# Optimization experiments

Hardware: AMD Instinct MI355X
Metric: run time of the kernel (lower is better)

## Reference

```python
import jax, jax.numpy as jnp
import numpy as np

NUM_HEADS = 32
HEAD_DIM = 32  # hard-coded in the module


def _rope_sincos(seq_len, head_dim):
    # NOTE: module uses arange(0, head_dim)/head_dim (full dim, not the usual /2 stride)
    inv_freq = 1.0 / (10000.0 ** (jnp.arange(0, head_dim, dtype=jnp.float32) / head_dim))
    freqs = jnp.outer(jnp.arange(seq_len, dtype=jnp.float32), inv_freq)  # [S, D]
    # original repeats over heads then reshapes -> identical values per head,
    # so broadcasting with shape [1, S, 1, D] is equivalent.
    return jnp.sin(freqs)[None, :, None, :], jnp.cos(freqs)[None, :, None, :]


def _apply_rope(x, sin, cos):
    x1, x2 = jnp.split(x, 2, axis=-1)
    x_rot = jnp.concatenate([-x2, x1], axis=-1)
    return x * cos + x_rot * sin


def setup_inputs() -> dict:
    key = jax.random.key(0)
    B, S, H, D = 2, 2048, NUM_HEADS, HEAD_DIM
    dm = H * D
    k1, k2 = jax.random.split(key)
    x = jax.random.normal(k1, (B, S, dm), dtype=jnp.float32)
    W_qkv = jax.random.normal(k2, (dm, 3 * dm), dtype=jnp.float32) / np.sqrt(dm).astype(np.float32)
    mask = jnp.tril(jnp.ones((S, S), dtype=bool))[None, None]  # causal, [1,1,S,S]
    return {"x": x, "W_qkv": W_qkv, "mask": mask}


def reference(x, W_qkv, mask):
    B, S, dm = x.shape
    H, D = NUM_HEADS, HEAD_DIM
    qkv = x @ W_qkv  # [B, S, 3*H*D], no bias
    q, k, v = jnp.split(qkv, 3, axis=-1)
    q = q.reshape(B, S, H, D)
    k = k.reshape(B, S, H, D)
    v = v.reshape(B, S, H, D)

    sin, cos = _rope_sincos(S, D)
    q = _apply_rope(q, sin, cos)
    k = _apply_rope(k, sin, cos)

    # [B, H, S, D]
    q = q.transpose(0, 2, 1, 3)
    k = k.transpose(0, 2, 1, 3)
    v = v.transpose(0, 2, 1, 3)

    scale = 1.0 / np.sqrt(D).astype(np.float32)
    attn = jnp.einsum('bhqd,bhkd->bhqk', q, k) * scale  # [B, H, S, S]
    attn = jnp.where(mask, attn, jnp.float32(-jnp.inf))
    attn = jax.nn.softmax(attn, axis=-1)
    out = jnp.einsum('bhqk,bhkd->bhqd', attn, v)  # [B, H, S, D]
    return out.transpose(0, 2, 1, 3).reshape(B, S, H * D)
```

## Files before the change

### kernel.cpp

```cpp
#include <hip/hip_runtime.h>
#include <cstdint>
#include <cstddef>

#define BB 2
#define SS 2048
#define HH 32
#define DD 32
#define DM 1024
#define MROWS 4096
#define NQKV 3072

#define QSCALE 0.25503486f

typedef __attribute__((ext_vector_type(8))) short bf16x8;
typedef __attribute__((ext_vector_type(4))) float f32x4;
typedef __attribute__((address_space(1))) unsigned int gu32;
typedef __attribute__((address_space(3))) unsigned int lu32;

__device__ __forceinline__ unsigned short f2bf(float f) {
    union { float f; unsigned int u; } v;
    v.f = f;
    unsigned int u = v.u;
    u += 0x7fffu + ((u >> 16) & 1u);
    return (unsigned short)(u >> 16);
}

__device__ __forceinline__ unsigned int cvt_pk_bf16(float a, float b) {
    unsigned int r;
    asm("v_cvt_pk_bf16_f32 %0, %1, %2" : "=v"(r) : "v"(a), "v"(b));
    return r;
}
__device__ __forceinline__ unsigned short bf1(float a) {
    return (unsigned short)cvt_pk_bf16(a, a);
}

__global__ __launch_bounds__(256) void prep_k(
        const float* __restrict__ x, const float* __restrict__ w,
        unsigned short* __restrict__ xb, unsigned short* __restrict__ wT,
        float* __restrict__ tk, float* __restrict__ tq) {
    __shared__ unsigned short tile[64][65];
    const int blk = blockIdx.x;
    const int tid = threadIdx.x;
    if (blk < 4096) {
        const int i = blk * 256 + tid;
        float4 v = ((const float4*)x)[i];
        ushort4 o;
        o.x = f2bf(v.x); o.y = f2bf(v.y); o.z = f2bf(v.z); o.w = f2bf(v.w);
        ((ushort4*)xb)[i] = o;
    } else if (blk < 4864) {
        const int bx = blk - 4096;
        const int n0 = (bx % 48) * 64;
        const int k0 = (bx / 48) * 64;
        const int tx = tid & 63;
        const int ty = tid >> 6;
        for (int i = ty; i < 64; i += 4)
            tile[i][tx] = f2bf(w[(size_t)(k0 + i) * NQKV + n0 + tx]);
        __syncthreads();
        for (int i = ty; i < 64; i += 4)
            wT[(size_t)(n0 + i) * 1024 + k0 + tx] = tile[tx][i];
    } else {
        const int i = (blk - 4864) * 256 + tid;
        const int s = i >> 4, dl = i & 15;
        const float inv1 = exp2f((float)dl * -0.41524101186092029f);
        const float inv2 = exp2f((float)(dl + 16) * -0.41524101186092029f);
        float s1, c1, s2, c2;
        sincosf((float)s * inv1, &s1, &c1);
        sincosf((float)s * inv2, &s2, &c2);
        float4 vk = {s1, c1, s2, c2};
        float4 vq = {s1 * QSCALE, c1 * QSCALE, s2 * QSCALE, c2 * QSCALE};
        ((float4*)tk)[i] = vk;
        ((float4*)tq)[i] = vq;
    }
}

__global__ __launch_bounds__(256) void qkv_gemm_k(
        const unsigned short* __restrict__ xb,
        const unsigned short* __restrict__ wTp,
        const float4* __restrict__ tk, const float4* __restrict__ tq,
        unsigned short* __restrict__ qbuf,
        unsigned short* __restrict__ kbuf,
        unsigned short* __restrict__ vtbuf) {
    __shared__ unsigned short smem[2 * 128 * 32];
    unsigned short* As = smem;
    unsigned short* Bs = smem + 4096;
    const int m0 = blockIdx.x * 128;
    const int n0 = blockIdx.y * 128;
    const int tid = threadIdx.x;
    const int w = tid >> 6, lane = tid & 63;
    const int quad = lane >> 4, l16 = lane & 15;
    const int wr = w >> 1, wc = w & 1;

    f32x4 acc[4][4];
#pragma unroll
    for (int i = 0; i < 4; ++i)
#pragma unroll
        for (int j = 0; j < 4; ++j)
            acc[i][j] = (f32x4){0.f, 0.f, 0.f, 0.f};

    const int G = (lane & 56) | ((lane ^ (lane >> 3)) & 7);
    const int goff = (G >> 2) * 1024 + (G & 3) * 8;
    const int Gr = l16 * 4 + quad;
    const int L = Gr ^ ((Gr >> 3) & 7);
    const int roff = L * 8;

    for (int k0 = 0; k0 < 1024; k0 += 32) {
        __syncthreads();
#pragma unroll
        for (int q = 0; q < 2; ++q) {
            const int seg = w * 2 + q;
            const unsigned short* ga = xb  + (size_t)(m0 + seg * 16) * 1024 + k0 + goff;
            const unsigned short* gb = wTp + (size_t)(n0 + seg * 16) * 1024 + k0 + goff;
            __builtin_amdgcn_global_load_lds((gu32*)ga, (lu32*)(As + seg * 512), 16, 0, 0);
            __builtin_amdgcn_global_load_lds((gu32*)gb, (lu32*)(Bs + seg * 512), 16, 0, 0);
        }
        __syncthreads();
        bf16x8 af[4], bfv[4];
#pragma unroll
        for (int i = 0; i < 4; ++i)
            af[i] = *(const bf16x8*)(As + (wr * 4 + i) * 512 + roff);
#pragma unroll
        for (int j = 0; j < 4; ++j)
            bfv[j] = *(const bf16x8*)(Bs + (wc * 4 + j) * 512 + roff);
#pragma unroll
        for (int i = 0; i < 4; ++i)
#pragma unroll
            for (int j = 0; j < 4; ++j)
                acc[i][j] = __builtin_amdgcn_mfma_f32_16x16x32_bf16(af[i], bfv[j], acc[i][j], 0, 0, 0);
    }

    const int sec = n0 >> 10;
    const int rowb = m0 + wr * 64;
    const int colb = n0 + wc * 64;
    if (sec < 2) {
        unsigned short* dst = (sec == 0) ? qbuf : kbuf;
        const float4* tab = (sec == 0) ? tq : tk;
        const int h0 = (colb & 1023) >> 5;
        const int h1 = ((colb + 32) & 1023) >> 5;
#pragma unroll
        for (int i = 0; i < 4; ++i) {
#pragma unroll
            for (int r = 0; r < 4; ++r) {
                const int row = rowb + i * 16 + quad * 4 + r;
                const int bb = row >> 11, s = row & 2047;
                const float4 t = tab[s * 16 + l16];
                unsigned short* pb = dst + ((size_t)(bb * 32) * 2048 + s) * 32;
                {
                    const float x1 = acc[i][0][r], x2 = acc[i][1][r];
                    unsigned short* p = pb + (size_t)h0 * (2048 * 32);
                    p[l16]      = bf1(x1 * t.y - x2 * t.x);
                    p[l16 + 16] = bf1(x2 * t.w + x1 * t.z);
                }
                {
                    const float x1 = acc[i][2][r], x2 = acc[i][3][r];
                    unsigned short* p = pb + (size_t)h1 * (2048 * 32);
                    p[l16]      = bf1(x1 * t.y - x2 * t.x);
                    p[l16 + 16] = bf1(x2 * t.w + x1 * t.z);
                }
            }
        }
    } else {
        __syncthreads();
        unsigned short* tw = smem + w * 2048;
        const int bbi = rowb >> 11;
        const int srow = rowb & 2047;
        const int colB = colb - 2048;
#pragma unroll
        for (int j = 0; j < 4; ++j) {
#pragma unroll
            for (int i = 0; i < 4; ++i) {
                uint2 pk;
                pk.x = cvt_pk_bf16(acc[i][j][0], acc[i][j][1]);
                pk.y = cvt_pk_bf16(acc[i][j][2], acc[i][j][3]);
                *(uint2*)&tw[l16 * 66 + i * 16 + quad * 4] = pk;
            }
#pragma unroll
            for (int c = 0; c < 16; ++c) {
                const int col = colB + j * 16 + c;
                const int hh = col >> 5, d = col & 31;
                vtbuf[((size_t)(bbi * 32 + hh) * 32 + d) * 2048 + srow + lane] = tw[c * 66 + lane];
            }
        }
    }
}

__global__ __launch_bounds__(256) void attn_k(
        const unsigned short* __restrict__ qb,
        const unsigned short* __restrict__ kb,
        const unsigned short* __restrict__ vt,
        float* __restrict__ out) {
    __shared__ unsigned short Pl[4][2][32][40];
    const int tid = threadIdx.x;
    const int w = tid >> 6, lane = tid & 63;
    const int quad = lane >> 4, l16 = lane & 15;
    const int bh = blockIdx.x >> 3;
    const int pr = blockIdx.x & 7;
    const int b = bh >> 5, h = bh & 31;

    const unsigned short* qbase = qb + (size_t)bh * 2048 * 32;
    const unsigned short* kbase = kb + (size_t)bh * 2048 * 32;
    const unsigned short* vbase = vt + (size_t)bh * 32 * 2048;
    const f32x4 fz = {0.f, 0.f, 0.f, 0.f};

    for (int ph = 0; ph < 2; ++ph) {
        const int qw = (ph == 0) ? (pr * 128 + w * 32)
                                 : ((15 - pr) * 128 + (3 - w) * 32);
        const int nkt = (qw >> 5) + 1;

        bf16x8 qf0 = *(const bf16x8*)(qbase + (size_t)(qw + l16) * 32 + quad * 8);
        bf16x8 qf1 = *(const bf16x8*)(qbase + (size_t)(qw + 16 + l16) * 32 + quad * 8);

        f32x4 a00 = fz, a01 = fz, a10 = fz, a11 = fz;
        float ls0 = 0.f, ls1 = 0.f;

        const unsigned short* kp0 = kbase + (size_t)l16 * 32 + quad * 8;
        const unsigned short* kp1 = kbase + (size_t)(16 + l16) * 32 + quad * 8;
        const unsigned short* vp0 = vbase + (size_t)l16 * 2048 + quad * 8;
        const unsigned short* vp1 = vbase + (size_t)(16 + l16) * 2048 + quad * 8;

        bf16x8 kc0 = *(const bf16x8*)kp0;
        bf16x8 kc1 = *(const bf16x8*)kp1;
        bf16x8 vc0 = *(const bf16x8*)vp0;
        bf16x8 vc1 = *(const bf16x8*)vp1;

        for (int kt = 0; kt < nkt - 1; ++kt) {
            kp0 += 1024; kp1 += 1024; vp0 += 32; vp1 += 32;
            bf16x8 kn0 = *(const bf16x8*)kp0;
            bf16x8 kn1 = *(const bf16x8*)kp1;
            bf16x8 vn0 = *(const bf16x8*)vp0;
            bf16x8 vn1 = *(const bf16x8*)vp1;

            f32x4 s00 = __builtin_amdgcn_mfma_f32_16x16x32_bf16(kc0, qf0, fz, 0, 0, 0);
            f32x4 s01 = __builtin_amdgcn_mfma_f32_16x16x32_bf16(kc0, qf1, fz, 0, 0, 0);
            f32x4 s10 = __builtin_amdgcn_mfma_f32_16x16x32_bf16(kc1, qf0, fz, 0, 0, 0);
            f32x4 s11 = __builtin_amdgcn_mfma_f32_16x16x32_bf16(kc1, qf1, fz, 0, 0, 0);

            unsigned short (*plw)[40] = Pl[w][kt & 1];
            {
                float p0 = __builtin_amdgcn_exp2f(s00[0]), p1 = __builtin_amdgcn_exp2f(s00[1]);
                float p2 = __builtin_amdgcn_exp2f(s00[2]), p3 = __builtin_amdgcn_exp2f(s00[3]);
                ls0 += (p0 + p1) + (p2 + p3);
                uint2 pk; pk.x = cvt_pk_bf16(p0, p1); pk.y = cvt_pk_bf16(p2, p3);
                *(uint2*)&plw[l16][quad * 4] = pk;
            }
            {
                float p0 = __builtin_amdgcn_exp2f(s01[0]), p1 = __builtin_amdgcn_exp2f(s01[1]);
                float p2 = __builtin_amdgcn_exp2f(s01[2]), p3 = __builtin_amdgcn_exp2f(s01[3]);
                ls1 += (p0 + p1) + (p2 + p3);
                uint2 pk; pk.x = cvt_pk_bf16(p0, p1); pk.y = cvt_pk_bf16(p2, p3);
                *(uint2*)&plw[16 + l16][quad * 4] = pk;
            }
            {
                float p0 = __builtin_amdgcn_exp2f(s10[0]), p1 = __builtin_amdgcn_exp2f(s10[1]);
                float p2 = __builtin_amdgcn_exp2f(s10[2]), p3 = __builtin_amdgcn_exp2f(s10[3]);
                ls0 += (p0 + p1) + (p2 + p3);
                uint2 pk; pk.x = cvt_pk_bf16(p0, p1); pk.y = cvt_pk_bf16(p2, p3);
                *(uint2*)&plw[l16][16 + quad * 4] = pk;
            }
            {
                float p0 = __builtin_amdgcn_exp2f(s11[0]), p1 = __builtin_amdgcn_exp2f(s11[1]);
                float p2 = __builtin_amdgcn_exp2f(s11[2]), p3 = __builtin_amdgcn_exp2f(s11[3]);
                ls1 += (p0 + p1) + (p2 + p3);
                uint2 pk; pk.x = cvt_pk_bf16(p0, p1); pk.y = cvt_pk_bf16(p2, p3);
                *(uint2*)&plw[16 + l16][16 + quad * 4] = pk;
            }

            bf16x8 pf0 = *(const bf16x8*)&plw[l16][quad * 8];
            bf16x8 pf1 = *(const bf16x8*)&plw[16 + l16][quad * 8];
            a00 = __builtin_amdgcn_mfma_f32_16x16x32_bf16(vc0, pf0, a00, 0, 0, 0);
            a01 = __builtin_amdgcn_mfma_f32_16x16x32_bf16(vc0, pf1, a01, 0, 0, 0);
            a10 = __builtin_amdgcn_mfma_f32_16x16x32_bf16(vc1, pf0, a10, 0, 0, 0);
            a11 = __builtin_amdgcn_mfma_f32_16x16x32_bf16(vc1, pf1, a11, 0, 0, 0);

            kc0 = kn0; kc1 = kn1; vc0 = vn0; vc1 = vn1;
        }

        {
            f32x4 s00 = __builtin_amdgcn_mfma_f32_16x16x32_bf16(kc0, qf0, fz, 0, 0, 0);
            f32x4 s01 = __builtin_amdgcn_mfma_f32_16x16x32_bf16(kc0, qf1, fz, 0, 0, 0);
            f32x4 s11 = __builtin_amdgcn_mfma_f32_16x16x32_bf16(kc1, qf1, fz, 0, 0, 0);

            unsigned short (*plw)[40] = Pl[w][(nkt - 1) & 1];
            {
                float p[4];
#pragma unroll
                for (int r = 0; r < 4; ++r)
                    p[r] = (quad * 4 + r > l16) ? 0.f : __builtin_amdgcn_exp2f(s00[r]);
                ls0 += (p[0] + p[1]) + (p[2] + p[3]);
                uint2 pk; pk.x = cvt_pk_bf16(p[0], p[1]); pk.y = cvt_pk_bf16(p[2], p[3]);
                *(uint2*)&plw[l16][quad * 4] = pk;
            }
            {
                float p0 = __builtin_amdgcn_exp2f(s01[0]), p1 = __builtin_amdgcn_exp2f(s01[1]);
                float p2 = __builtin_amdgcn_exp2f(s01[2]), p3 = __builtin_amdgcn_exp2f(s01[3]);
                ls1 += (p0 + p1) + (p2 + p3);
                uint2 pk; pk.x = cvt_pk_bf16(p0, p1); pk.y = cvt_pk_bf16(p2, p3);
                *(uint2*)&plw[16 + l16][quad * 4] = pk;
            }
            {
                uint2 pk; pk.x = 0; pk.y = 0;
                *(uint2*)&plw[l16][16 + quad * 4] = pk;
            }
            {
                float p[4];
#pragma unroll
                for (int r = 0; r < 4; ++r)
                    p[r] = (quad * 4 + r > l16) ? 0.f : __builtin_amdgcn_exp2f(s11[r]);
                ls1 += (p[0] + p[1]) + (p[2] + p[3]);
                uint2 pk; pk.x = cvt_pk_bf16(p[0], p[1]); pk.y = cvt_pk_bf16(p[2], p[3]);
                *(uint2*)&plw[16 + l16][16 + quad * 4] = pk;
            }

            bf16x8 pf0 = *(const bf16x8*)&plw[l16][quad * 8];
            bf16x8 pf1 = *(const bf16x8*)&plw[16 + l16][quad * 8];
            a00 = __builtin_amdgcn_mfma_f32_16x16x32_bf16(vc0, pf0, a00, 0, 0, 0);
            a01 = __builtin_amdgcn_mfma_f32_16x16x32_bf16(vc0, pf1, a01, 0, 0, 0);
            a10 = __builtin_amdgcn_mfma_f32_16x16x32_bf16(vc1, pf0, a10, 0, 0, 0);
            a11 = __builtin_amdgcn_mfma_f32_16x16x32_bf16(vc1, pf1, a11, 0, 0, 0);
        }

        float l0 = ls0; l0 += __shfl_xor(l0, 16); l0 += __shfl_xor(l0, 32);
        float l1 = ls1; l1 += __shfl_xor(l1, 16); l1 += __shfl_xor(l1, 32);
        const float inv0 = 1.f / l0, inv1 = 1.f / l1;

        float* ot = (float*)&Pl[w][0][0][0];
        {
            f32x4 t;
            t = a00; t[0]*=inv0; t[1]*=inv0; t[2]*=inv0; t[3]*=inv0;
            *(f32x4*)&ot[(l16) * 36 + quad * 4] = t;
            t = a10; t[0]*=inv0; t[1]*=inv0; t[2]*=inv0; t[3]*=inv0;
            *(f32x4*)&ot[(l16) * 36 + 16 + quad * 4] = t;
            t = a01; t[0]*=inv1; t[1]*=inv1; t[2]*=inv1; t[3]*=inv1;
            *(f32x4*)&ot[(16 + l16) * 36 + quad * 4] = t;
            t = a11; t[0]*=inv1; t[1]*=inv1; t[2]*=inv1; t[3]*=inv1;
            *(f32x4*)&ot[(16 + l16) * 36 + 16 + quad * 4] = t;
        }
        const int dd = lane & 31, qpar = lane >> 5;
        float* ob = out + (size_t)(b * 2048 + qw) * 1024 + h * 32;
#pragma unroll
        for (int i2 = 0; i2 < 16; ++i2) {
            const int qloc = i2 * 2 + qpar;
            ob[(size_t)qloc * 1024 + dd] = ot[qloc * 36 + dd];
        }
    }
}

extern "C" void kernel_launch(void* const* d_in, const int* in_sizes, int n_in,
                              void* d_out, int out_size, void* d_ws, size_t ws_size,
                              hipStream_t stream) {
    (void)in_sizes; (void)n_in; (void)out_size; (void)ws_size;
    const float* x = (const float*)d_in[0];
    const float* wq = (const float*)d_in[1];
    float* out = (float*)d_out;

    unsigned short* xb = (unsigned short*)d_ws;
    unsigned short* wT = xb + (size_t)MROWS * DM;
    unsigned short* qb = wT + (size_t)NQKV * DM;
    unsigned short* kb = qb + (size_t)BB * HH * SS * DD;
    unsigned short* vt = kb + (size_t)BB * HH * SS * DD;
    float* tk = (float*)(vt + (size_t)BB * HH * SS * DD);
    float* tq = tk + (size_t)SS * 16 * 4;

    prep_k<<<dim3(4992), dim3(256), 0, stream>>>(x, wq, xb, wT, tk, tq);
    qkv_gemm_k<<<dim3(MROWS / 128, NQKV / 128), dim3(256), 0, stream>>>(
        xb, wT, (const float4*)tk, (const float4*)tq, qb, kb, vt);
    attn_k<<<dim3(BB * HH * 8), dim3(256), 0, stream>>>(qb, kb, vt, out);
}
```

Baseline: 182.3 us.

## Keep P in registers via 16-row query tiles, dropping LDS round-trip

```diff
diff --git a/kernel.cpp b/kernel.cpp
--- a/kernel.cpp
+++ b/kernel.cpp
@@ -188,159 +188,129 @@
         const unsigned short* __restrict__ kb,
         const unsigned short* __restrict__ vt,
         float* __restrict__ out) {
-    __shared__ unsigned short Pl[4][2][32][40];
     const int tid = threadIdx.x;
     const int w = tid >> 6, lane = tid & 63;
     const int quad = lane >> 4, l16 = lane & 15;
-    const int bh = blockIdx.x >> 3;
-    const int pr = blockIdx.x & 7;
+    const int bh = blockIdx.x >> 4;
+    const int pr = blockIdx.x & 15;
     const int b = bh >> 5, h = bh & 31;
+    const int W = pr * 4 + w;
 
     const unsigned short* qbase = qb + (size_t)bh * 2048 * 32;
     const unsigned short* kbase = kb + (size_t)bh * 2048 * 32;
     const unsigned short* vbase = vt + (size_t)bh * 32 * 2048;
     const f32x4 fz = {0.f, 0.f, 0.f, 0.f};
 
+    typedef union { unsigned int u[4]; uint2 d[2]; bf16x8 v; } pk8;
+
     for (int ph = 0; ph < 2; ++ph) {
-        const int qw = (ph == 0) ? (pr * 128 + w * 32)
-                                 : ((15 - pr) * 128 + (3 - w) * 32);
+        const int j = (ph == 0) ? W : (127 - W);
+        const int qw = j * 16;
         const int nkt = (qw >> 5) + 1;
 
-        bf16x8 qf0 = *(const bf16x8*)(qbase + (size_t)(qw + l16) * 32 + quad * 8);
-        bf16x8 qf1 = *(const bf16x8*)(qbase + (size_t)(qw + 16 + l16) * 32 + quad * 8);
-
-        f32x4 a00 = fz, a01 = fz, a10 = fz, a11 = fz;
-        float ls0 = 0.f, ls1 = 0.f;
+        bf16x8 qf = *(const bf16x8*)(qbase + (size_t)(qw + l16) * 32 + quad * 8);
+
+        f32x4 a0 = fz, a1 = fz;
+        float ls = 0.f;
 
         const unsigned short* kp0 = kbase + (size_t)l16 * 32 + quad * 8;
         const unsigned short* kp1 = kbase + (size_t)(16 + l16) * 32 + quad * 8;
-        const unsigned short* vp0 = vbase + (size_t)l16 * 2048 + quad * 8;
-        const unsigned short* vp1 = vbase + (size_t)(16 + l16) * 2048 + quad * 8;
+        const unsigned short* vq0 = vbase + (size_t)l16 * 2048 + quad * 4;
+        const unsigned short* vq1 = vbase + (size_t)(16 + l16) * 2048 + quad * 4;
 
         bf16x8 kc0 = *(const bf16x8*)kp0;
         bf16x8 kc1 = *(const bf16x8*)kp1;
-        bf16x8 vc0 = *(const bf16x8*)vp0;
-        bf16x8 vc1 = *(const bf16x8*)vp1;
+        uint2 v00 = *(const uint2*)vq0;
+        uint2 v01 = *(const uint2*)(vq0 + 16);
+        uint2 v10 = *(const uint2*)vq1;
+        uint2 v11 = *(const uint2*)(vq1 + 16);
 
         for (int kt = 0; kt < nkt - 1; ++kt) {
-            kp0 += 1024; kp1 += 1024; vp0 += 32; vp1 += 32;
+            kp0 += 1024; kp1 += 1024; vq0 += 32; vq1 += 32;
             bf16x8 kn0 = *(const bf16x8*)kp0;
             bf16x8 kn1 = *(const bf16x8*)kp1;
-            bf16x8 vn0 = *(const bf16x8*)vp0;
-            bf16x8 vn1 = *(const bf16x8*)vp1;
-
-            f32x4 s00 = __builtin_amdgcn_mfma_f32_16x16x32_bf16(kc0, qf0, fz, 0, 0, 0);
-            f32x4 s01 = __builtin_amdgcn_mfma_f32_16x16x32_bf16(kc0, qf1, fz, 0, 0, 0);
-            f32x4 s10 = __builtin_amdgcn_mfma_f32_16x16x32_bf16(kc1, qf0, fz, 0, 0, 0);
-            f32x4 s11 = __builtin_amdgcn_mfma_f32_16x16x32_bf16(kc1, qf1, fz, 0, 0, 0);
-
-            unsigned short (*plw)[40] = Pl[w][kt & 1];
+            uint2 n00 = *(const uint2*)vq0;
+            uint2 n01 = *(const uint2*)(vq0 + 16);
+            uint2 n10 = *(const uint2*)vq1;
+            uint2 n11 = *(const uint2*)(vq1 + 16);
+
+            f32x4 s0 = __builtin_amdgcn_mfma_f32_16x16x32_bf16(kc0, qf, fz, 0, 0, 0);
+            f32x4 s1 = __builtin_amdgcn_mfma_f32_16x16x32_bf16(kc1, qf, fz, 0, 0, 0);
+
+            pk8 pf;
             {
-                float p0 = __builtin_amdgcn_exp2f(s00[0]), p1 = __builtin_amdgcn_exp2f(s00[1]);
-                float p2 = __builtin_amdgcn_exp2f(s00[2]), p3 = __builtin_amdgcn_exp2f(s00[3]);
-                ls0 += (p0 + p1) + (p2 + p3);
-                uint2 pk; pk.x = cvt_pk_bf16(p0, p1); pk.y = cvt_pk_bf16(p2, p3);
-                *(uint2*)&plw[l16][quad * 4] = pk;
+                float p0 = __builtin_amdgcn_exp2f(s0[0]), p1 = __builtin_amdgcn_exp2f(s0[1]);
+                float p2 = __builtin_amdgcn_exp2f(s0[2]), p3 = __builtin_amdgcn_exp2f(s0[3]);
+                ls += (p0 + p1) + (p2 + p3);
+                pf.u[0] = cvt_pk_bf16(p0, p1);
+                pf.u[1] = cvt_pk_bf16(p2, p3);
             }
             {
-                float p0 = __builtin_amdgcn_exp2f(s01[0]), p1 = __builtin_amdgcn_exp2f(s01[1]);
-                float p2 = __builtin_amdgcn_exp2f(s01[2]), p3 = __builtin_amdgcn_exp2f(s01[3]);
-                ls1 += (p0 + p1) + (p2 + p3);
-                uint2 pk; pk.x = cvt_pk_bf16(p0, p1); pk.y = cvt_pk_bf16(p2, p3);
-                *(uint2*)&plw[16 + l16][quad * 4] = pk;
-            }
-            {
-                float p0 = __builtin_amdgcn_exp2f(s10[0]), p1 = __builtin_amdgcn_exp2f(s10[1]);
-                float p2 = __builtin_amdgcn_exp2f(s10[2]), p3 = __builtin_amdgcn_exp2f(s10[3]);
-                ls0 += (p0 + p1) + (p2 + p3);
-                uint2 pk; pk.x = cvt_pk_bf16(p0, p1); pk.y = cvt_pk_bf16(p2, p3);
-                *(uint2*)&plw[l16][16 + quad * 4] = pk;
-            }
-            {
-                float p0 = __builtin_amdgcn_exp2f(s11[0]), p1 = __builtin_amdgcn_exp2f(s11[1]);
-                float p2 = __builtin_amdgcn_exp2f(s11[2]), p3 = __builtin_amdgcn_exp2f(s11[3]);
-                ls1 += (p0 + p1) + (p2 + p3);
-                uint2 pk; pk.x = cvt_pk_bf16(p0, p1); pk.y = cvt_pk_bf16(p2, p3);
-                *(uint2*)&plw[16 + l16][16 + quad * 4] = pk;
-            }
-
-            bf16x8 pf0 = *(const bf16x8*)&plw[l16][quad * 8];
-            bf16x8 pf1 = *(const bf16x8*)&plw[16 + l16][quad * 8];
-            a00 = __builtin_amdgcn_mfma_f32_16x16x32_bf16(vc0, pf0, a00, 0, 0, 0);
-            a01 = __builtin_amdgcn_mfma_f32_16x16x32_bf16(vc0, pf1, a01, 0, 0, 0);
-            a10 = __builtin_amdgcn_mfma_f32_16x16x32_bf16(vc1, pf0, a10, 0, 0, 0);
-            a11 = __builtin_amdgcn_mfma_f32_16x16x32_bf16(vc1, pf1, a11, 0, 0, 0);
-
-            kc0 = kn0; kc1 = kn1; vc0 = vn0; vc1 = vn1;
+                float p0 = __builtin_amdgcn_exp2f(s1[0]), p1 = __builtin_amdgcn_exp2f(s1[1]);
+                float p2 = __builtin_amdgcn_exp2f(s1[2]), p3 = __builtin_amdgcn_exp2f(s1[3]);
+                ls += (p0 + p1) + (p2 + p3);
+                pf.u[2] = cvt_pk_bf16(p0, p1);
+                pf.u[3] = cvt_pk_bf16(p2, p3);
+            }
+            pk8 vc0, vc1;
+            vc0.d[0] = v00; vc0.d[1] = v01;
+            vc1.d[0] = v10; vc1.d[1] = v11;
+            a0 = __builtin_amdgcn_mfma_f32_16x16x32_bf16(vc0.v, pf.v, a0, 0, 0, 0);
+            a1 = __builtin_amdgcn_mfma_f32_16x16x32_bf16(vc1.v, pf.v, a1, 0, 0, 0);
+
+            kc0 = kn0; kc1 = kn1; v00 = n00; v01 = n01; v10 = n10; v11 = n11;
         }
 
         {
-            f32x4 s00 = __builtin_amdgcn_mfma_f32_16x16x32_bf16(kc0, qf0, fz, 0, 0, 0);
-            f32x4 s01 = __builtin_amdgcn_mfma_f32_16x16x32_bf16(kc0, qf1, fz, 0, 0, 0);
-            f32x4 s11 = __builtin_amdgcn_mfma_f32_16x16x32_bf16(kc1, qf1, fz, 0, 0, 0);
-
-            unsigned short (*plw)[40] = Pl[w][(nkt - 1) & 1];
-            {
+            f32x4 s0 = __builtin_amdgcn_mfma_f32_16x16x32_bf16(kc0, qf, fz, 0, 0, 0);
+            pk8 pf;
+            if (j & 1) {
+                f32x4 s1 = __builtin_amdgcn_mfma_f32_16x16x32_bf16(kc1, qf, fz, 0, 0, 0);
+                {
+                    float p0 = __builtin_amdgcn_exp2f(s0[0]), p1 = __builtin_amdgcn_exp2f(s0[1]);
+                    float p2 = __builtin_amdgcn_exp2f(s0[2]), p3 = __builtin_amdgcn_exp2f(s0[3]);
+                    ls += (p0 + p1) + (p2 + p3);
+                    pf.u[0] = cvt_pk_bf16(p0, p1);
+                    pf.u[1] = cvt_pk_bf16(p2, p3);
+                }
+                {
+                    float p[4];
+#pragma unroll
+                    for (int r = 0; r < 4; ++r)
+                        p[r] = (quad * 4 + r > l16) ? 0.f : __builtin_amdgcn_exp2f(s1[r]);
+                    ls += (p[0] + p[1]) + (p[2] + p[3]);
+                    pf.u[2] = cvt_pk_bf16(p[0], p[1]);
+                    pf.u[3] = cvt_pk_bf16(p[2], p[3]);
+                }
+            } else {
                 float p[4];
 #pragma unroll
                 for (int r = 0; r < 4; ++r)
-                    p[r] = (quad * 4 + r > l16) ? 0.f : __builtin_amdgcn_exp2f(s00[r]);
-                ls0 += (p[0] + p[1]) + (p[2] + p[3]);
-                uint2 pk; pk.x = cvt_pk_bf16(p[0], p[1]); pk.y = cvt_pk_bf16(p[2], p[3]);
-                *(uint2*)&plw[l16][quad * 4] = pk;
-            }
-            {
-                float p0 = __builtin_amdgcn_exp2f(s01[0]), p1 = __builtin_amdgcn_exp2f(s01[1]);
-                float p2 = __builtin_amdgcn_exp2f(s01[2]), p3 = __builtin_amdgcn_exp2f(s01[3]);
-                ls1 += (p0 + p1) + (p2 + p3);
-                uint2 pk; pk.x = cvt_pk_bf16(p0, p1); pk.y = cvt_pk_bf16(p2, p3);
-                *(uint2*)&plw[16 + l16][quad * 4] = pk;
-            }
-            {
-                uint2 pk; pk.x = 0; pk.y = 0;
-                *(uint2*)&plw[l16][16 + quad * 4] = pk;
-            }
-            {
-                float p[4];
-#pragma unroll
-                for (int r = 0; r < 4; ++r)
-                    p[r] = (quad * 4 + r > l16) ? 0.f : __builtin_amdgcn_exp2f(s11[r]);
-                ls1 += (p[0] + p[1]) + (p[2] + p[3]);
-                uint2 pk; pk.x = cvt_pk_bf16(p[0], p[1]); pk.y = cvt_pk_bf16(p[2], p[3]);
-                *(uint2*)&plw[16 + l16][16 + quad * 4] = pk;
-            }
-
-            bf16x8 pf0 = *(const bf16x8*)&plw[l16][quad * 8];
-            bf16x8 pf1 = *(const bf16x8*)&plw[16 + l16][quad * 8];
-            a00 = __builtin_amdgcn_mfma_f32_16x16x32_bf16(vc0, pf0, a00, 0, 0, 0);
-            a01 = __builtin_amdgcn_mfma_f32_16x16x32_bf16(vc0, pf1, a01, 0, 0, 0);
-            a10 = __builtin_amdgcn_mfma_f32_16x16x32_bf16(vc1, pf0, a10, 0, 0, 0);
-            a11 = __builtin_amdgcn_mfma_f32_16x16x32_bf16(vc1, pf1, a11, 0, 0, 0);
-        }
-
-        float l0 = ls0; l0 += __shfl_xor(l0, 16); l0 += __shfl_xor(l0, 32);
-        float l1 = ls1; l1 += __shfl_xor(l1, 16); l1 += __shfl_xor(l1, 32);
-        const float inv0 = 1.f / l0, inv1 = 1.f / l1;
-
-        float* ot = (float*)&Pl[w][0][0][0];
-        {
-            f32x4 t;
-            t = a00; t[0]*=inv0; t[1]*=inv0; t[2]*=inv0; t[3]*=inv0;
-            *(f32x4*)&ot[(l16) * 36 + quad * 4] = t;
-            t = a10; t[0]*=inv0; t[1]*=inv0; t[2]*=inv0; t[3]*=inv0;
-            *(f32x4*)&ot[(l16) * 36 + 16 + quad * 4] = t;
-            t = a01; t[0]*=inv1; t[1]*=inv1; t[2]*=inv1; t[3]*=inv1;
-            *(f32x4*)&ot[(16 + l16) * 36 + quad * 4] = t;
-            t = a11; t[0]*=inv1; t[1]*=inv1; t[2]*=inv1; t[3]*=inv1;
-            *(f32x4*)&ot[(16 + l16) * 36 + 16 + quad * 4] = t;
-        }
-        const int dd = lane & 31, qpar = lane >> 5;
-        float* ob = out + (size_t)(b * 2048 + qw) * 1024 + h * 32;
-#pragma unroll
-        for (int i2 = 0; i2 < 16; ++i2) {
-            const int qloc = i2 * 2 + qpar;
-            ob[(size_t)qloc * 1024 + dd] = ot[qloc * 36 + dd];
-        }
+                    p[r] = (quad * 4 + r > l16) ? 0.f : __builtin_amdgcn_exp2f(s0[r]);
+                ls += (p[0] + p[1]) + (p[2] + p[3]);
+                pf.u[0] = cvt_pk_bf16(p[0], p[1]);
+                pf.u[1] = cvt_pk_bf16(p[2], p[3]);
+                pf.u[2] = 0;
+                pf.u[3] = 0;
+            }
+            pk8 vc0, vc1;
+            vc0.d[0] = v00; vc0.d[1] = v01;
+            vc1.d[0] = v10; vc1.d[1] = v11;
+            a0 = __builtin_amdgcn_mfma_f32_16x16x32_bf16(vc0.v, pf.v, a0, 0, 0, 0);
+            a1 = __builtin_amdgcn_mfma_f32_16x16x32_bf16(vc1.v, pf.v, a1, 0, 0, 0);
+        }
+
+        float l = ls;
+        l += __shfl_xor(l, 16);
+        l += __shfl_xor(l, 32);
+        const float inv = 1.f / l;
+
+        float* ob = out + (size_t)(b * 2048 + qw + l16) * 1024 + h * 32 + quad * 4;
+        float4 o0, o1;
+        o0.x = a0[0] * inv; o0.y = a0[1] * inv; o0.z = a0[2] * inv; o0.w = a0[3] * inv;
+        o1.x = a1[0] * inv; o1.y = a1[1] * inv; o1.z = a1[2] * inv; o1.w = a1[3] * inv;
+        *(float4*)ob = o0;
+        *(float4*)(ob + 16) = o1;
     }
 }
 
@@ -363,5 +333,5 @@
     prep_k<<<dim3(4992), dim3(256), 0, stream>>>(x, wq, xb, wT, tk, tq);
     qkv_gemm_k<<<dim3(MROWS / 128, NQKV / 128), dim3(256), 0, stream>>>(
         xb, wT, (const float4*)tk, (const float4*)tq, qb, kb, vt);
-    attn_k<<<dim3(BB * HH * 8), dim3(256), 0, stream>>>(qb, kb, vt, out);
-}
+    attn_k<<<dim3(BB * HH * 16), dim3(256), 0, stream>>>(qb, kb, vt, out);
+}
```

New measurement: 276.0 us. 51.4% more time.
